# Optimization experiments

Measured on AMD Instinct MI355X. Metric: run time of the kernel, lower is better.

The kernel has to match this reference:

```python
import jax, jax.numpy as jnp
import numpy as np

NUM_FREQS = 96
FRAME_SIZE = 5


def setup_inputs() -> dict:
    key = jax.random.key(0)
    k1, k2 = jax.random.split(key)
    B, T, F = 8, 4096, 481
    spec = jax.random.normal(k1, (B, 1, T, F, 2), dtype=jnp.float32)
    coefs = jax.random.normal(k2, (B, FRAME_SIZE, T, NUM_FREQS, 2), dtype=jnp.float32)
    return {"spec": spec, "coefs": coefs}


def reference(spec, coefs):
    # spec: [B,1,T,F,2], coefs: [B,O,T,Fdf,2] with O == FRAME_SIZE, Fdf == NUM_FREQS
    fs, nf = FRAME_SIZE, NUM_FREQS
    T = spec.shape[2]

    spec_df = spec[:, :, :, :nf, :]                      # [B,1,T,Fdf,2]
    padded = jnp.pad(spec_df, ((0, 0), (0, 0), (fs - 1, 0), (0, 0), (0, 0)))
    # causal sliding window indices over time
    win_idx = jnp.arange(T)[:, None] + jnp.arange(fs)[None, :]  # [T,fs]
    unfolded = padded[:, :, win_idx]                     # [B,1,T,fs,Fdf,2]
    u = jnp.transpose(unfolded, (0, 1, 2, 4, 3, 5))      # [B,1,T,Fdf,fs,2]

    c = jnp.transpose(coefs[:, None], (0, 1, 3, 4, 2, 5))  # [B,1,T,Fdf,O,2]

    s_re, s_im = u[..., 0], u[..., 1]
    c_re, c_im = c[..., 0], c[..., 1]
    out_re = jnp.sum(s_re * c_re - s_im * c_im, axis=-1)  # [B,1,T,Fdf]
    out_im = jnp.sum(s_re * c_im + s_im * c_re, axis=-1)
    spec_f = jnp.stack([out_re, out_im], axis=-1)          # [B,1,T,Fdf,2]

    spec_hi = spec[:, :, :, nf:, :]
    return jnp.concatenate([spec_f, spec_hi], axis=3)      # [B,1,T,F,2]
```

## Files before the change

### kernel.cpp

```cpp
#include <hip/hip_runtime.h>

#define BB 8
#define TT 4096
#define FF 481
#define NF 96
#define FS 5

__global__ __launch_bounds__(256) void df_kernel(
    const float2* __restrict__ spec,
    const float2* __restrict__ coefs,
    float2* __restrict__ out)
{
    const int f = blockIdx.x * 256 + threadIdx.x;
    const int t = blockIdx.y;
    const int b = blockIdx.z;
    if (f >= FF) return;

    const long long sidx = ((long long)b * TT + t) * FF + f;

    if (f >= NF) {
        out[sidx] = spec[sidx];
        return;
    }

    float acc_re = 0.f, acc_im = 0.f;
#pragma unroll
    for (int i = 0; i < FS; ++i) {
        const int ts = t + i - (FS - 1);
        if (ts < 0) continue;
        const float2 s = spec[((long long)b * TT + ts) * FF + f];
        const float2 c = coefs[(((long long)b * FS + i) * TT + t) * NF + f];
        acc_re = fmaf(s.x, c.x, acc_re);
        acc_re = fmaf(-s.y, c.y, acc_re);
        acc_im = fmaf(s.x, c.y, acc_im);
        acc_im = fmaf(s.y, c.x, acc_im);
    }

    float2 r; r.x = acc_re; r.y = acc_im;
    out[sidx] = r;
}

extern "C" void kernel_launch(void* const* d_in, const int* in_sizes, int n_in,
                              void* d_out, int out_size, void* d_ws, size_t ws_size,
                              hipStream_t stream) {
    const float2* spec  = (const float2*)d_in[0];
    const float2* coefs = (const float2*)d_in[1];
    float2* out = (float2*)d_out;

    dim3 grid((FF + 255) / 256, TT, BB);
    df_kernel<<<grid, dim3(256), 0, stream>>>(spec, coefs, out);
}
```

Measured before the change: 337.4 us.

## Split work into dense filter and copy partitions with grid-stride loops

```diff
diff --git a/kernel.cpp b/kernel.cpp
--- a/kernel.cpp
+++ b/kernel.cpp
@@ -6,38 +6,50 @@
 #define NF 96
 #define FS 5
 
-__global__ __launch_bounds__(256) void df_kernel(
+#define N_FILT (BB * TT * NF)
+#define N_HI   (BB * TT * (FF - NF))
+#define NBLK   4096
+#define FB     1920
+
+__global__ __launch_bounds__(256) void df_all(
     const float2* __restrict__ spec,
     const float2* __restrict__ coefs,
     float2* __restrict__ out)
 {
-    const int f = blockIdx.x * 256 + threadIdx.x;
-    const int t = blockIdx.y;
-    const int b = blockIdx.z;
-    if (f >= FF) return;
+    const unsigned bid = blockIdx.x;
 
-    const long long sidx = ((long long)b * TT + t) * FF + f;
+    if (bid < FB) {
+        const unsigned stride = FB * 256u;
+        for (unsigned n = bid * 256u + threadIdx.x; n < (unsigned)N_FILT; n += stride) {
+            const unsigned f  = n % (unsigned)NF;
+            const unsigned bt = n / (unsigned)NF;
+            const unsigned t  = bt & (TT - 1u);
+            const unsigned b  = bt >> 12;
 
-    if (f >= NF) {
-        out[sidx] = spec[sidx];
-        return;
+            float accx = 0.f, accy = 0.f;
+#pragma unroll
+            for (int i = 0; i < FS; ++i) {
+                const int ts = (int)t + i - (FS - 1);
+                if (ts < 0) continue;
+                const float2 s = spec[(b * TT + (unsigned)ts) * FF + f];
+                const float2 c = coefs[((b * FS + (unsigned)i) * TT + t) * NF + f];
+                accx = fmaf(s.x, c.x, accx);
+                accx = fmaf(-s.y, c.y, accx);
+                accy = fmaf(s.x, c.y, accy);
+                accy = fmaf(s.y, c.x, accy);
+            }
+            float2 r; r.x = accx; r.y = accy;
+            out[bt * FF + f] = r;
+        }
+    } else {
+        const unsigned stride = (NBLK - FB) * 256u;
+        for (unsigned n = (bid - FB) * 256u + threadIdx.x; n < (unsigned)N_HI; n += stride) {
+            const unsigned p  = n % (unsigned)(FF - NF);
+            const unsigned bt = n / (unsigned)(FF - NF);
+            const unsigned idx = bt * FF + NF + p;
+            out[idx] = spec[idx];
+        }
     }
-
-    float acc_re = 0.f, acc_im = 0.f;
-#pragma unroll
-    for (int i = 0; i < FS; ++i) {
-        const int ts = t + i - (FS - 1);
-        if (ts < 0) continue;
-        const float2 s = spec[((long long)b * TT + ts) * FF + f];
-        const float2 c = coefs[(((long long)b * FS + i) * TT + t) * NF + f];
-        acc_re = fmaf(s.x, c.x, acc_re);
-        acc_re = fmaf(-s.y, c.y, acc_re);
-        acc_im = fmaf(s.x, c.y, acc_im);
-        acc_im = fmaf(s.y, c.x, acc_im);
-    }
-
-    float2 r; r.x = acc_re; r.y = acc_im;
-    out[sidx] = r;
 }
 
 extern "C" void kernel_launch(void* const* d_in, const int* in_sizes, int n_in,
@@ -47,6 +59,5 @@
     const float2* coefs = (const float2*)d_in[1];
     float2* out = (float2*)d_out;
 
-    dim3 grid((FF + 255) / 256, TT, BB);
-    df_kernel<<<grid, dim3(256), 0, stream>>>(spec, coefs, out);
+    df_all<<<dim3(NBLK), dim3(256), 0, stream>>>(spec, coefs, out);
 }
```

Result: faster. 303.3 us (-10.1%).
